# Performance work log

Hardware: AMD Instinct MI355X
Metric: run time of the kernel (lower is better)

Reference implementation:

```python
import jax, jax.numpy as jnp
import numpy as np


def _conv1x1(x, w, b):
    # x: (B,Ci,H,W), w: (Co,Ci) -> (B,Co,H,W)
    return jnp.einsum('bchw,oc->bohw', x, w) + b[None, :, None, None]


def _conv3x3(x, w, b):
    # x: (B,Ci,H,W), w: (Co,Ci,3,3), stride 1, padding 1 ('SAME')
    y = jax.lax.conv_general_dilated(
        x, w, window_strides=(1, 1), padding='SAME',
        dimension_numbers=('NCHW', 'OIHW', 'NCHW'))
    return y + b[None, :, None, None]


def setup_inputs() -> dict:
    key = jax.random.key(0)
    ks = jax.random.split(key, 10)
    N, B, Cc, Cf, H, W = 3, 8, 128, 256, 64, 64
    s = 0.05  # weight scale to keep attention logits well-conditioned
    return {
        'contexts': jax.random.normal(ks[0], (N, B, Cc, 2 * H, 2 * W), jnp.float32),
        'mainstream': jax.random.normal(ks[1], (B, Cf, H, W), jnp.float32),
        'Wc_w': jax.random.normal(ks[2], (Cc, Cc), jnp.float32) * s,
        'Wc_b': jax.random.normal(ks[3], (Cc,), jnp.float32) * s,
        'Wf_w': jax.random.normal(ks[4], (Cc, Cf), jnp.float32) * s,
        'Wf_b': jax.random.normal(ks[5], (Cc,), jnp.float32) * s,
        'Wk_w': jax.random.normal(ks[6], (Cc, Cf), jnp.float32) * s,
        'Wk_b': jax.random.normal(ks[7], (Cc,), jnp.float32) * s,
        'Wv_w': jax.random.normal(ks[8], (Cc, Cf, 3, 3), jnp.float32) * s,
        'Wv_b': jax.random.normal(ks[9], (Cc,), jnp.float32) * s,
    }


def reference(contexts, mainstream, Wc_w, Wc_b, Wf_w, Wf_b, Wk_w, Wk_b, Wv_w, Wv_b):
    N, B, Cc = contexts.shape[0], contexts.shape[1], contexts.shape[2]
    H, W = mainstream.shape[2], mainstream.shape[3]

    q = _conv1x1(mainstream, Wf_w, Wf_b)        # (B,Cc,H,W) queries
    mkey = _conv1x1(mainstream, Wk_w, Wk_b)     # (B,Cc,H,W) mainline keys
    vals = _conv3x3(mainstream, Wv_w, Wv_b)     # (B,Cc,H,W) mainline values
    ckeys = jax.vmap(lambda c: _conv1x1(c, Wc_w, Wc_b))(contexts)  # (N,B,Cc,2H,2W)

    # unfold 2x2 sub-pixel blocks: (.., 2H, 2W) -> (.., H, 2, W, 2)
    ckeys = ckeys.reshape(N, B, Cc, H, 2, W, 2)
    cfeat = contexts.reshape(N, B, Cc, H, 2, W, 2)

    # per-pixel cross-attention logits: context keys . query
    logits_ctx = jnp.einsum('nbchiwj,bchw->nbhiwj', ckeys, q)      # (N,B,H,2,W,2)
    # mainline key . query (same logit for all 4 sub-pixels)
    logit_main = jnp.einsum('bchw,bchw->bhw', mkey, q)[None, :, :, None, :, None]
    logits = jnp.concatenate(
        [logits_ctx, jnp.broadcast_to(logit_main, (1, B, H, 2, W, 2))], axis=0)

    attn = jax.nn.softmax(logits, axis=0)                          # (N+1,B,H,2,W,2)

    vfeat = jnp.broadcast_to(vals[None, :, :, :, None, :, None],
                             (1, B, Cc, H, 2, W, 2))
    feats = jnp.concatenate([cfeat, vfeat], axis=0)                # (N+1,B,Cc,H,2,W,2)

    out = jnp.einsum('nbhiwj,nbchiwj->bchiwj', attn, feats)        # (B,Cc,H,2,W,2)
    return out.reshape(B, Cc, 2 * H, 2 * W)
```

## Files before the change

kernel.cpp:

```cpp
#include <hip/hip_runtime.h>

#define NCTX 3
#define B 8
#define CC 128
#define CF 256
#define H 64
#define W 64
#define HW 4096
#define YX 16384

#define WS_QT    0
#define WS_VALS  4194304
#define WS_BIAS  8388608
#define WS_LM    8421376
#define WS_WALL  8454144
#define WS_MSP   8552960
#define WS_WB    13013504
#define WS_WALLO 13160960

typedef __attribute__((ext_vector_type(8))) short bf16x8;
typedef __attribute__((ext_vector_type(4))) float f32x4;
typedef __attribute__((ext_vector_type(8))) unsigned short u16x8;

__device__ __forceinline__ unsigned short f2b(float f) {
    union { float f; unsigned u; } c; c.f = f;
    unsigned u = c.u + 0x7FFFu + ((c.u >> 16) & 1u);
    return (unsigned short)(u >> 16);
}
__device__ __forceinline__ float b2f(unsigned short u) {
    union { unsigned u; float f; } c; c.u = ((unsigned)u) << 16;
    return c.f;
}

__global__ __launch_bounds__(256) void k0(
    const float* __restrict__ Wc_w, const float* __restrict__ Wc_b,
    const float* __restrict__ Wf_w, const float* __restrict__ Wf_b,
    const float* __restrict__ Wk_w, const float* __restrict__ Wk_b,
    const float* __restrict__ Wv, const float* __restrict__ ms,
    unsigned short* __restrict__ Wall, unsigned short* __restrict__ Wallo,
    float* __restrict__ bias448, unsigned short* __restrict__ Wb,
    unsigned short* __restrict__ msP) {
    __shared__ float Ls[32][65];
    int blk = blockIdx.x;
    int t = threadIdx.x;
    if (blk < 448) {
        int o = blk * 256 + t;
        int ci8 = o & 7;
        int idx = o >> 3;
        int row = idx % 448;
        int sc4 = idx / 448;
        int f = (sc4 >> 2) * 32 + (sc4 & 3) * 8 + ci8;
        float w;
        if (row < 128) {
            float s = 0.f;
            for (int o2 = 0; o2 < 128; ++o2) s += Wc_w[o2 * 128 + row] * Wf_w[o2 * 256 + f];
            w = s;
        } else if (row < 384) {
            int p = (row - 128) >> 1;
            w = (row & 1) ? Wk_w[p * 256 + f] : Wf_w[p * 256 + f];
        } else if (row == 384) {
            float s = 0.f;
            for (int o2 = 0; o2 < 128; ++o2) s += Wc_b[o2] * Wf_w[o2 * 256 + f];
            w = s;
        } else w = 0.f;
        unsigned short hi = f2b(w);
        Wall[o] = hi;
        Wallo[o] = f2b(w - b2f(hi));
        if (o < 448) {
            float bb;
            if (o < 128) {
                float s = 0.f;
                for (int o2 = 0; o2 < 128; ++o2) s += Wc_w[o2 * 128 + o] * Wf_b[o2];
                bb = s;
            } else if (o < 384) {
                int p = (o - 128) >> 1;
                bb = (o & 1) ? Wk_b[p] : Wf_b[p];
            } else if (o == 384) {
                float s = 0.f;
                for (int o2 = 0; o2 < 128; ++o2) s += Wc_b[o2] * Wf_b[o2];
                bb = s;
            } else if (o == 385) bb = -1.f;
            else bb = 0.f;
            bias448[o] = bb;
        }
    } else if (blk < 1600) {
        int o = (blk - 448) * 256 + t;
        int ci8 = o & 7;
        int co  = (o >> 3) & 127;
        int c4  = (o >> 10) & 3;
        int s   = (o >> 12) & 7;
        int khw = o >> 15;
        int ci  = s * 32 + c4 * 8 + ci8;
        int kh  = khw / 3, kw = khw - kh * 3;
        Wb[o] = f2b(Wv[((co * 256 + ci) * 3 + kh) * 3 + kw]);
    } else if (blk < 1860) {
        int i = (blk - 1600) * 256 + t;
        if (i < 66560) {
            size_t off;
            if (i < 33792) {
                int x = i % 66; int r = i / 66;
                int g = r & 31, rowi = (r >> 5) & 1, b = r >> 6;
                off = ((((size_t)b * 66 + rowi * 65) * 32) + g) * 66 + x;
            } else {
                int k = i - 33792;
                int xi = k & 1; int g = (k >> 1) & 31; int y1 = (k >> 6) & 63; int b = k >> 12;
                off = ((((size_t)b * 66 + (y1 + 1)) * 32) + g) * 66 + xi * 65;
            }
            *(u16x8*)&msP[off * 8] = (u16x8){0, 0, 0, 0, 0, 0, 0, 0};
        }
    } else {
        int local = blk - 1860;
        int s = local & 7;
        int h = (local >> 3) & 63;
        int b = local >> 9;
        const float* src = ms + ((size_t)b * 256 + s * 32) * HW + h * 64;
        for (int l = t; l < 2048; l += 256) {
            int ci = l >> 6, w = l & 63;
            Ls[ci][w] = src[ci * HW + w];
        }
        __syncthreads();
        int w = t & 63, gi = t >> 6;
        u16x8 vh;
#pragma unroll
        for (int j = 0; j < 8; ++j) vh[j] = f2b(Ls[gi * 8 + j][w]);
        size_t offH = ((((size_t)b * 66 + (h + 1)) * 32) + (s * 4 + gi)) * 66 + (w + 1);
        *(u16x8*)&msP[offH * 8] = vh;
    }
}

__global__ __launch_bounds__(512, 4) void kmm(
    const float* __restrict__ ms, const unsigned short* __restrict__ msP,
    const unsigned short* __restrict__ Wall, const unsigned short* __restrict__ Wallo,
    const float* __restrict__ bias448, const unsigned short* __restrict__ Wb,
    const float* __restrict__ Wv_b,
    unsigned short* __restrict__ qtB, float* __restrict__ lm,
    unsigned short* __restrict__ valsB) {
    __shared__ unsigned char smem[25856] __attribute__((aligned(16)));
    int t = threadIdx.x;
    int lane = t & 63, wid = t >> 6;
    int c4l = lane >> 4, lrow = lane & 15;
    int blk = blockIdx.x;

    if (blk < 512) {
        auto Bs = (unsigned short (*)[2][4][64][8])smem;
        float* biasS = (float*)(smem + 16384);
        float* lmAcc = (float*)(smem + 16384 + 1792);
        int wm = wid >> 1, wn = wid & 1;
        int b = blk >> 6, h = blk & 63;
        int xs = t & 63, g4 = t >> 6;
        int c4w = g4 >> 1, sub = g4 & 1;
        const float* msb = ms + ((size_t)b * 256 + g4 * 4) * HW + h * 64 + xs;
        for (int i = t; i < 448; i += 512) biasS[i] = bias448[i];
        if (t < 64) lmAcc[t] = 0.f;

        f32x4 acc[7][2];
#pragma unroll
        for (int mf = 0; mf < 7; ++mf)
#pragma unroll
            for (int nf = 0; nf < 2; ++nf) acc[mf][nf] = (f32x4){0.f, 0.f, 0.f, 0.f};

        const bf16x8* Whip = (const bf16x8*)Wall;
        const bf16x8* Wlop = (const bf16x8*)Wallo;

#define CVT_WRITE(bufv, F0, F1, F2, F3) do {                                    \
        unsigned short h0 = f2b(F0), h1 = f2b(F1), h2 = f2b(F2), h3 = f2b(F3);  \
        unsigned short q0 = f2b((F0) - b2f(h0)), q1 = f2b((F1) - b2f(h1));      \
        unsigned short q2 = f2b((F2) - b2f(h2)), q3 = f2b((F3) - b2f(h3));      \
        uint2 hw, lw;                                                           \
        hw.x = (unsigned)h0 | ((unsigned)h1 << 16);                             \
        hw.y = (unsigned)h2 | ((unsigned)h3 << 16);                             \
        lw.x = (unsigned)q0 | ((unsigned)q1 << 16);                             \
        lw.y = (unsigned)q2 | ((unsigned)q3 << 16);                             \
        *(uint2*)&Bs[bufv][0][c4w][xs][sub * 4] = hw;                           \
        *(uint2*)&Bs[bufv][1][c4w][xs][sub * 4] = lw;                           \
    } while (0)

        {
            float f0 = msb[0], f1 = msb[HW], f2 = msb[2 * HW], f3 = msb[3 * HW];
            CVT_WRITE(0, f0, f1, f2, f3);
        }
        __syncthreads();

        for (int s = 0; s < 8; ++s) {
            int cur = s & 1;
            float fn0, fn1, fn2, fn3;
            if (s < 7) {
                const float* p = msb + (size_t)(s + 1) * 32 * HW;
                fn0 = p[0]; fn1 = p[HW]; fn2 = p[2 * HW]; fn3 = p[3 * HW];
            }
            bf16x8 bh[2], bl[2];
#pragma unroll
            for (int nf = 0; nf < 2; ++nf) {
                int x = wn * 32 + nf * 16 + lrow;
                bh[nf] = *(const bf16x8*)&Bs[cur][0][c4l][x][0];
                bl[nf] = *(const bf16x8*)&Bs[cur][1][c4l][x][0];
            }
#pragma unroll
            for (int mf = 0; mf < 7; ++mf) {
                size_t widx = (size_t)(s * 4 + c4l) * 448 + wm * 112 + mf * 16 + lrow;
                bf16x8 ah = Whip[widx];
                bf16x8 al = Wlop[widx];
#pragma unroll
                for (int nf = 0; nf < 2; ++nf) {
                    acc[mf][nf] = __builtin_amdgcn_mfma_f32_16x16x32_bf16(ah, bh[nf], acc[mf][nf], 0, 0, 0);
                    acc[mf][nf] = __builtin_amdgcn_mfma_f32_16x16x32_bf16(ah, bl[nf], acc[mf][nf], 0, 0, 0);
                    acc[mf][nf] = __builtin_amdgcn_mfma_f32_16x16x32_bf16(al, bh[nf], acc[mf][nf], 0, 0, 0);
                }
            }
            if (s < 7) CVT_WRITE(cur ^ 1, fn0, fn1, fn2, fn3);
            __syncthreads();
        }
#undef CVT_WRITE

        int px0 = wn * 32;
        float lmp[2] = {0.f, 0.f};
#pragma unroll
        for (int mf = 0; mf < 7; ++mf) {
            int base = wm * 112 + mf * 16;
            int r0 = base + c4l * 4;
            if (base < 128) {
#pragma unroll
                for (int nf = 0; nf < 2; ++nf) {
                    int x = px0 + nf * 16 + lrow;
                    unsigned short* dst = qtB + ((size_t)b * 128 + r0) * HW + h * 64 + x;
                    f32x4 v = acc[mf][nf];
#pragma unroll
                    for (int j = 0; j < 4; ++j)
                        dst[(size_t)j * HW] = f2b(v[j] + biasS[r0 + j]);
                }
            } else {
                float b0 = biasS[r0], b1 = biasS[r0 + 1], b2 = biasS[r0 + 2], b3 = biasS[r0 + 3];
#pragma unroll
                for (int nf = 0; nf < 2; ++nf) {
                    f32x4 v = acc[mf][nf];
                    lmp[nf] += (v[0] + b0) * (v[1] + b1) + (v[2] + b2) * (v[3] + b3);
                }
            }
        }
        if (wm != 0) {
#pragma unroll
            for (int nf = 0; nf < 2; ++nf) {
                lmp[nf] += __shfl_xor(lmp[nf], 16);
                lmp[nf] += __shfl_xor(lmp[nf], 32);
            }
            if (c4l == 0) {
#pragma unroll
                for (int nf = 0; nf < 2; ++nf)
                    atomicAdd(&lmAcc[px0 + nf * 16 + lrow], lmp[nf]);
            }
        }
        __syncthreads();
        if (t < 64) lm[b * HW + h * 64 + t] = lmAcc[t];
    } else {
        auto Bs = (unsigned short (*)[6336])smem;
        float* biasS = (float*)(smem + 25344);
        int local = blk - 512;
        int b = local >> 6;
        int hl = local & 63;
        int h = ((hl & 7) << 3) | (hl >> 3);
        int wm = wid >> 1, wn = wid & 1;
        if (t < 128) biasS[t] = Wv_b[t];

        f32x4 acc[2][2];
#pragma unroll
        for (int mf = 0; mf < 2; ++mf)
#pragma unroll
            for (int nf = 0; nf < 2; ++nf) acc[mf][nf] = (f32x4){0.f, 0.f, 0.f, 0.f};

        const bf16x8* Wbp = (const bf16x8*)Wb;

#define STAGE2(bufv, sv) do {                                                       \
        for (int iter = 0; iter < 2; ++iter) {                                      \
            int q0 = iter * 512 + (wid << 6);                                       \
            int q = q0 + lane;                                                      \
            if (q < 792) {                                                          \
                int rc = q / 66; int x = q - rc * 66;                               \
                int r = rc >> 2, c4 = rc & 3;                                       \
                int y = h + r;                               \
                const unsigned short* gp = msP +                                    \
                    (((((size_t)b * 66 + y) * 32) + ((sv) * 4 + c4)) * 66 + x) * 8; \
                unsigned short* lp = &Bs[bufv][q0 * 8];                             \
                __builtin_amdgcn_global_load_lds(                                   \
                    (const __attribute__((address_space(1))) void*)gp,              \
                    (__attribute__((address_space(3))) void*)lp, 16, 0, 0);         \
            }                                                                       \
        }                                                                           \
    } while (0)

        STAGE2(0, 0);
        __syncthreads();

        for (int s = 0; s < 8; ++s) {
            int cur = s & 1;
            if (s < 7) STAGE2(cur ^ 1, s + 1);
#pragma unroll
            for (int khw = 0; khw < 9; ++khw) {
                int kh = khw / 3, kw = khw - 3 * (khw / 3);
                bf16x8 a[2];
#pragma unroll
                for (int mf = 0; mf < 2; ++mf)
                    a[mf] = Wbp[((khw * 8 + s) * 4 + c4l) * 128 + wm * 32 + mf * 16 + lrow];
                bf16x8 bf[2];
#pragma unroll
                for (int nf = 0; nf < 2; ++nf) {
                    int chunk = (kh * 4 + c4l) * 66 + wn * 32 + nf * 16 + lrow + kw;
                    bf[nf] = *(const bf16x8*)&Bs[cur][chunk * 8];
                }
#pragma unroll
                for (int mf = 0; mf < 2; ++mf)
#pragma unroll
                    for (int nf = 0; nf < 2; ++nf)
                        acc[mf][nf] = __builtin_amdgcn_mfma_f32_16x16x32_bf16(
                            a[mf], bf[nf], acc[mf][nf], 0, 0, 0);
            }
            __syncthreads();
        }
#undef STAGE2

#pragma unroll
        for (int mf = 0; mf < 2; ++mf) {
            int co0 = wm * 32 + mf * 16 + c4l * 4;
#pragma unroll
            for (int nf = 0; nf < 2; ++nf) {
                int x = wn * 32 + nf * 16 + lrow;
                unsigned short* dst = valsB + (((size_t)b * 128 + co0) * HW) + h * 64 + x;
                f32x4 v = acc[mf][nf];
#pragma unroll
                for (int j = 0; j < 4; ++j)
                    dst[(size_t)j * HW] = f2b(v[j] + biasS[co0 + j]);
            }
        }
    }
}

__global__ __launch_bounds__(256, 4) void k3(
    const float* __restrict__ ctx, const unsigned short* __restrict__ qtB,
    const unsigned short* __restrict__ valsB, const float* __restrict__ lm,
    float* __restrict__ out) {
    __shared__ float part[4][3][64];
    __shared__ float attnS[4][64];
    int t = threadIdx.x;
    int lane = t & 63, wv = t >> 6;
    int xg = t & 15, cq = t >> 4;
    int blk0 = blockIdx.x;
    int blk = (blk0 & 7) * 256 + (blk0 >> 3);
    int b = blk >> 8, y = (blk >> 1) & 127, xh = blk & 1;
    int h = y >> 1;
    int x0 = xh * 64 + xg * 4;
    int p0 = xh * 32 + xg * 2;

    const unsigned short* qb = qtB + ((size_t)b * 128 + cq * 8) * HW + h * 64 + p0;
    unsigned qvp[8];
#pragma unroll
    for (int j = 0; j < 8; ++j) qvp[j] = *(const unsigned*)&qb[(size_t)j * HW];

    float4 cx[3][8];
#pragma unroll
    for (int n = 0; n < 3; ++n) {
        const float* cb = ctx + ((size_t)(n * 8 + b) * 128 + cq * 8) * YX + (size_t)y * 128 + x0;
#pragma unroll
        for (int j = 0; j < 8; ++j) cx[n][j] = *(const float4*)&cb[(size_t)j * YX];
    }
#pragma unroll
    for (int n = 0; n < 3; ++n) {
        float lp[4] = {0.f, 0.f, 0.f, 0.f};
#pragma unroll
        for (int j = 0; j < 8; ++j) {
            float qx = b2f((unsigned short)(qvp[j] & 0xffffu));
            float qy = b2f((unsigned short)(qvp[j] >> 16));
            lp[0] += cx[n][j].x * qx;
            lp[1] += cx[n][j].y * qx;
            lp[2] += cx[n][j].z * qy;
            lp[3] += cx[n][j].w * qy;
        }
#pragma unroll
        for (int xl = 0; xl < 4; ++xl) {
            float v = lp[xl];
            v += __shfl_xor(v, 16);
            v += __shfl_xor(v, 32);
            lp[xl] = v;
        }
        if (lane < 16) {
#pragma unroll
            for (int xl = 0; xl < 4; ++xl)
                part[wv][n][lane * 4 + xl] = lp[xl];
        }
    }
    __syncthreads();
    if (t < 64) {
        float l0 = part[0][0][t] + part[1][0][t] + part[2][0][t] + part[3][0][t];
        float l1 = part[0][1][t] + part[1][1][t] + part[2][1][t] + part[3][1][t];
        float l2 = part[0][2][t] + part[1][2][t] + part[2][2][t] + part[3][2][t];
        float l3 = lm[(size_t)b * HW + h * 64 + xh * 32 + (t >> 1)];
        float m = fmaxf(fmaxf(l0, l1), fmaxf(l2, l3));
        float e0 = __expf(l0 - m), e1 = __expf(l1 - m), e2 = __expf(l2 - m), e3 = __expf(l3 - m);
        float inv = 1.f / (e0 + e1 + e2 + e3);
        attnS[0][t] = e0 * inv; attnS[1][t] = e1 * inv;
        attnS[2][t] = e2 * inv; attnS[3][t] = e3 * inv;
    }
    __syncthreads();
    const unsigned short* vb = valsB + ((size_t)b * 128 + cq * 8) * HW + h * 64 + p0;
    unsigned vvp[8];
#pragma unroll
    for (int j = 0; j < 8; ++j) vvp[j] = *(const unsigned*)&vb[(size_t)j * HW];
    float a0[4], a1[4], a2[4], a3[4];
#pragma unroll
    for (int xl = 0; xl < 4; ++xl) {
        a0[xl] = attnS[0][xg * 4 + xl];
        a1[xl] = attnS[1][xg * 4 + xl];
        a2[xl] = attnS[2][xg * 4 + xl];
        a3[xl] = attnS[3][xg * 4 + xl];
    }
    float* obase = out + ((size_t)b * 128 + cq * 8) * YX + (size_t)y * 128 + x0;
#pragma unroll
    for (int j = 0; j < 8; ++j) {
        float vx = b2f((unsigned short)(vvp[j] & 0xffffu));
        float vy = b2f((unsigned short)(vvp[j] >> 16));
        float4 o;
        o.x = a3[0] * vx + a0[0] * cx[0][j].x + a1[0] * cx[1][j].x + a2[0] * cx[2][j].x;
        o.y = a3[1] * vx + a0[1] * cx[0][j].y + a1[1] * cx[1][j].y + a2[1] * cx[2][j].y;
        o.z = a3[2] * vy + a0[2] * cx[0][j].z + a1[2] * cx[1][j].z + a2[2] * cx[2][j].z;
        o.w = a3[3] * vy + a0[3] * cx[0][j].w + a1[3] * cx[1][j].w + a2[3] * cx[2][j].w;
        *(float4*)&obase[(size_t)j * YX] = o;
    }
}

extern "C" void kernel_launch(void* const* d_in, const int* in_sizes, int n_in,
                              void* d_out, int out_size, void* d_ws, size_t ws_size,
                              hipStream_t stream) {
    const float* ctx  = (const float*)d_in[0];
    const float* ms   = (const float*)d_in[1];
    const float* Wc_w = (const float*)d_in[2];
    const float* Wc_b = (const float*)d_in[3];
    const float* Wf_w = (const float*)d_in[4];
    const float* Wf_b = (const float*)d_in[5];
    const float* Wk_w = (const float*)d_in[6];
    const float* Wk_b = (const float*)d_in[7];
    const float* Wv_w = (const float*)d_in[8];
    const float* Wv_b = (const float*)d_in[9];
    float* out = (float*)d_out;
    float* ws = (float*)d_ws;
    float* bias448 = ws + WS_BIAS;
    float* lmp     = ws + WS_LM;
    unsigned short* qtBp   = (unsigned short*)(ws + WS_QT);
    unsigned short* valsBp = (unsigned short*)(ws + WS_VALS);
    unsigned short* Wallp  = (unsigned short*)(ws + WS_WALL);
    unsigned short* Wallop = (unsigned short*)(ws + WS_WALLO);
    unsigned short* msPp   = (unsigned short*)(ws + WS_MSP);
    unsigned short* Wbp    = (unsigned short*)(ws + WS_WB);

    hipLaunchKernelGGL(k0, dim3(5956), dim3(256), 0, stream, Wc_w, Wc_b, Wf_w, Wf_b,
                       Wk_w, Wk_b, Wv_w, ms, Wallp, Wallop, bias448, Wbp, msPp);
    hipLaunchKernelGGL(kmm, dim3(1024), dim3(512), 0, stream, ms, msPp, Wallp, Wallop,
                       bias448, Wbp, Wv_b, qtBp, lmp, valsBp);
    hipLaunchKernelGGL(k3, dim3(2048), dim3(256), 0, stream, ctx, qtBp, valsBp, lmp, out);
}
```

Measured before the change: 157.9 us.

## Use online softmax over contexts in k3 to cut register pressure

Kernel k3 no longer keeps all three context tiles (96 floats per thread) live in registers. It processes one context at a time with an online-softmax running max and sum, folding each context into a float4 accumulator that is initialised from the mainline values. This lowers VGPR use and may raise occupancy. In exchange it adds two block barriers per context, serialises the context loads behind those barriers (unroll 1), and does extra exp work per thread.

```diff
diff --git a/kernel.cpp b/kernel.cpp
--- a/kernel.cpp
+++ b/kernel.cpp
@@ -337,8 +337,8 @@
     const float* __restrict__ ctx, const unsigned short* __restrict__ qtB,
     const unsigned short* __restrict__ valsB, const float* __restrict__ lm,
     float* __restrict__ out) {
-    __shared__ float part[4][3][64];
-    __shared__ float attnS[4][64];
+    __shared__ float part[4][64];
+    __shared__ float logitS[64];
     int t = threadIdx.x;
     int lane = t & 63, wv = t >> 6;
     int xg = t & 15, cq = t >> 4;
@@ -354,24 +354,35 @@
 #pragma unroll
     for (int j = 0; j < 8; ++j) qvp[j] = *(const unsigned*)&qb[(size_t)j * HW];
 
-    float4 cx[3][8];
-#pragma unroll
+    float lm0 = lm[(size_t)b * HW + h * 64 + p0];
+    float lm1 = lm[(size_t)b * HW + h * 64 + p0 + 1];
+    float m[4] = {lm0, lm0, lm1, lm1};
+    float sum[4] = {1.f, 1.f, 1.f, 1.f};
+    const unsigned short* vb = valsB + ((size_t)b * 128 + cq * 8) * HW + h * 64 + p0;
+    float4 oa[8];
+#pragma unroll
+    for (int j = 0; j < 8; ++j) {
+        unsigned v = *(const unsigned*)&vb[(size_t)j * HW];
+        float vx = b2f((unsigned short)(v & 0xffffu));
+        float vy = b2f((unsigned short)(v >> 16));
+        oa[j] = (float4){vx, vx, vy, vy};
+    }
+
+#pragma unroll 1
     for (int n = 0; n < 3; ++n) {
         const float* cb = ctx + ((size_t)(n * 8 + b) * 128 + cq * 8) * YX + (size_t)y * 128 + x0;
-#pragma unroll
-        for (int j = 0; j < 8; ++j) cx[n][j] = *(const float4*)&cb[(size_t)j * YX];
-    }
-#pragma unroll
-    for (int n = 0; n < 3; ++n) {
+        float4 cx[8];
+#pragma unroll
+        for (int j = 0; j < 8; ++j) cx[j] = *(const float4*)&cb[(size_t)j * YX];
         float lp[4] = {0.f, 0.f, 0.f, 0.f};
 #pragma unroll
         for (int j = 0; j < 8; ++j) {
             float qx = b2f((unsigned short)(qvp[j] & 0xffffu));
             float qy = b2f((unsigned short)(qvp[j] >> 16));
-            lp[0] += cx[n][j].x * qx;
-            lp[1] += cx[n][j].y * qx;
-            lp[2] += cx[n][j].z * qy;
-            lp[3] += cx[n][j].w * qy;
+            lp[0] += cx[j].x * qx;
+            lp[1] += cx[j].y * qx;
+            lp[2] += cx[j].z * qy;
+            lp[3] += cx[j].w * qy;
         }
 #pragma unroll
         for (int xl = 0; xl < 4; ++xl) {
@@ -382,45 +393,39 @@
         }
         if (lane < 16) {
 #pragma unroll
-            for (int xl = 0; xl < 4; ++xl)
-                part[wv][n][lane * 4 + xl] = lp[xl];
+            for (int xl = 0; xl < 4; ++xl) part[wv][lane * 4 + xl] = lp[xl];
+        }
+        __syncthreads();
+        if (t < 64) logitS[t] = part[0][t] + part[1][t] + part[2][t] + part[3][t];
+        __syncthreads();
+        float f[4], e[4];
+#pragma unroll
+        for (int xl = 0; xl < 4; ++xl) {
+            float ln = logitS[xg * 4 + xl];
+            float nm = fmaxf(m[xl], ln);
+            f[xl] = __expf(m[xl] - nm);
+            e[xl] = __expf(ln - nm);
+            sum[xl] = sum[xl] * f[xl] + e[xl];
+            m[xl] = nm;
+        }
+#pragma unroll
+        for (int j = 0; j < 8; ++j) {
+            oa[j].x = oa[j].x * f[0] + e[0] * cx[j].x;
+            oa[j].y = oa[j].y * f[1] + e[1] * cx[j].y;
+            oa[j].z = oa[j].z * f[2] + e[2] * cx[j].z;
+            oa[j].w = oa[j].w * f[3] + e[3] * cx[j].w;
         }
     }
-    __syncthreads();
-    if (t < 64) {
-        float l0 = part[0][0][t] + part[1][0][t] + part[2][0][t] + part[3][0][t];
-        float l1 = part[0][1][t] + part[1][1][t] + part[2][1][t] + part[3][1][t];
-        float l2 = part[0][2][t] + part[1][2][t] + part[2][2][t] + part[3][2][t];
-        float l3 = lm[(size_t)b * HW + h * 64 + xh * 32 + (t >> 1)];
-        float m = fmaxf(fmaxf(l0, l1), fmaxf(l2, l3));
-        float e0 = __expf(l0 - m), e1 = __expf(l1 - m), e2 = __expf(l2 - m), e3 = __expf(l3 - m);
-        float inv = 1.f / (e0 + e1 + e2 + e3);
-        attnS[0][t] = e0 * inv; attnS[1][t] = e1 * inv;
-        attnS[2][t] = e2 * inv; attnS[3][t] = e3 * inv;
-    }
-    __syncthreads();
-    const unsigned short* vb = valsB + ((size_t)b * 128 + cq * 8) * HW + h * 64 + p0;
-    unsigned vvp[8];
-#pragma unroll
-    for (int j = 0; j < 8; ++j) vvp[j] = *(const unsigned*)&vb[(size_t)j * HW];
-    float a0[4], a1[4], a2[4], a3[4];
-#pragma unroll
-    for (int xl = 0; xl < 4; ++xl) {
-        a0[xl] = attnS[0][xg * 4 + xl];
-        a1[xl] = attnS[1][xg * 4 + xl];
-        a2[xl] = attnS[2][xg * 4 + xl];
-        a3[xl] = attnS[3][xg * 4 + xl];
-    }
+
+    float r0 = 1.f / sum[0], r1 = 1.f / sum[1], r2 = 1.f / sum[2], r3 = 1.f / sum[3];
     float* obase = out + ((size_t)b * 128 + cq * 8) * YX + (size_t)y * 128 + x0;
 #pragma unroll
     for (int j = 0; j < 8; ++j) {
-        float vx = b2f((unsigned short)(vvp[j] & 0xffffu));
-        float vy = b2f((unsigned short)(vvp[j] >> 16));
         float4 o;
-        o.x = a3[0] * vx + a0[0] * cx[0][j].x + a1[0] * cx[1][j].x + a2[0] * cx[2][j].x;
-        o.y = a3[1] * vx + a0[1] * cx[0][j].y + a1[1] * cx[1][j].y + a2[1] * cx[2][j].y;
-        o.z = a3[2] * vy + a0[2] * cx[0][j].z + a1[2] * cx[1][j].z + a2[2] * cx[2][j].z;
-        o.w = a3[3] * vy + a0[3] * cx[0][j].w + a1[3] * cx[1][j].w + a2[3] * cx[2][j].w;
+        o.x = oa[j].x * r0;
+        o.y = oa[j].y * r1;
+        o.z = oa[j].z * r2;
+        o.w = oa[j].w * r3;
         *(float4*)&obase[(size_t)j * YX] = o;
     }
 }
```

After: 143.8 us. 8.9% less time.
